# Kernel tuning notes

Hardware: AMD Instinct MI355X
Metric: run time of the kernel (lower is better)

Reference implementation:

```python
import jax, jax.numpy as jnp
import numpy as np

B, S, P = 256, 1024, 4096   # batch, n_sensors, n_points
NM, H, PD = 64, 128, 128    # n_modes, hidden width, p
C = 1.0                     # speed of light param


def setup_inputs() -> dict:
    key = jax.random.key(0)
    ks = jax.random.split(key, 16)
    w = lambda k, shp: (jax.random.normal(k, shp, jnp.float32) * 0.05)
    return {
        "u0": jax.random.normal(ks[0], (B, S), jnp.float32),
        "x": jax.random.uniform(ks[1], (P,), jnp.float32, -1.0, 1.0),
        "t": jax.random.uniform(ks[2], (P,), jnp.float32, 0.0, 1.0),
        # branch MLP: (2*NM)->128->128->PD
        "bw1": w(ks[3], (H, 2 * NM)), "bb1": jnp.zeros((H,), jnp.float32),
        "bw2": w(ks[4], (H, H)),      "bb2": jnp.zeros((H,), jnp.float32),
        "bw3": w(ks[5], (PD, H)),     "bb3": jnp.zeros((PD,), jnp.float32),
        # trunk MLP: 4->128->128->PD
        "tw1": w(ks[6], (H, 4)),      "tb1": jnp.zeros((H,), jnp.float32),
        "tw2": w(ks[7], (H, H)),      "tb2": jnp.zeros((H,), jnp.float32),
        "tw3": w(ks[8], (PD, H)),     "tb3": jnp.zeros((PD,), jnp.float32),
    }


def _mlp(a, w1, b1, w2, b2, w3, b3):
    a = jax.nn.relu(a @ w1.T + b1)
    a = jax.nn.relu(a @ w2.T + b2)
    return a @ w3.T + b3


def reference(u0, x, t, bw1, bb1, bw2, bb2, bw3, bb3, tw1, tb1, tw2, tb2, tw3, tb3):
    # Fourier coefficients: mean over sensors of u0 * cos/sin(pi*k*xs)
    xs = jnp.linspace(-1.0, 1.0, S, dtype=jnp.float32)          # (S,)
    modes = jnp.arange(1, NM + 1, dtype=jnp.float32)            # (NM,)
    ang = jnp.pi * modes[:, None] * xs[None, :]                 # (NM, S)
    cos_c = (u0 @ jnp.cos(ang).T) / S                           # (B, NM)
    sin_c = (u0 @ jnp.sin(ang).T) / S                           # (B, NM)
    fourier = jnp.concatenate([cos_c, sin_c], axis=1)           # (B, 2*NM)

    branch_out = _mlp(fourier, bw1, bb1, bw2, bb2, bw3, bb3)    # (B, PD)

    xe = jnp.broadcast_to(x[None, :], (u0.shape[0], P))         # (B, P)
    te = jnp.broadcast_to(t[None, :], (u0.shape[0], P))
    pt_sq = te ** 2 - xe ** 2 / (C ** 2)
    # safe sqrt of clamp(pt_sq, min=0)
    proper_time = jnp.sqrt(jnp.where(pt_sq > 0, pt_sq, 0.0) + 0.0)
    causal = (jnp.abs(xe) <= C * te).astype(jnp.float32)
    trunk_feat = jnp.stack([xe, te, proper_time, causal], axis=-1)  # (B, P, 4)

    trunk_out = _mlp(trunk_feat, tw1, tb1, tw2, tb2, tw3, tb3)      # (B, P, PD)

    u_pred = jnp.einsum("bd,bpd->bp", branch_out, trunk_out)        # (B, P)
    return u_pred * causal
```

## Files before the change

### kernel.cpp

```cpp
#include <hip/hip_runtime.h>
#include <hip/hip_fp16.h>
#include <math.h>

#define NMODES 64
#define SDIM   1024
#define BATCH  256
#define PDIM   4096
#define HDIM   128

typedef _Float16 half8  __attribute__((ext_vector_type(8)));
typedef _Float16 half4v __attribute__((ext_vector_type(4)));
typedef float    f32x4  __attribute__((ext_vector_type(4)));

#define WSB_BRANCH 0
#define WSB_T3     (BATCH * HDIM * 2)

#define LDW 136

union KMixSmem {
    struct {
        _Float16 Ws[128 * LDW];
        _Float16 h1[32 * LDW];
        _Float16 h2[32 * LDW];
        float    feat[32][4];
    } tr;
    struct {
        float u0row[SDIM];
        float part[2][HDIM];
        float fr[HDIM];
        float hh[HDIM];
        float g2[HDIM];
    } fb;
};

__global__ __launch_bounds__(256) void k_mix(
    const float* __restrict__ u0,
    const float* __restrict__ xv, const float* __restrict__ tv,
    const float* __restrict__ bw1, const float* __restrict__ bb1,
    const float* __restrict__ bw2, const float* __restrict__ bb2,
    const float* __restrict__ bw3, const float* __restrict__ bb3,
    const float* __restrict__ tw1, const float* __restrict__ tb1,
    const float* __restrict__ tw2, const float* __restrict__ tb2,
    const float* __restrict__ tw3, const float* __restrict__ tb3,
    __half* __restrict__ branch_out, __half* __restrict__ t3g) {
    __shared__ KMixSmem sm;
    const int t = threadIdx.x;

    if (blockIdx.x < 128) {
        const int pbase = blockIdx.x * 32;

#pragma unroll
        for (int i = 0; i < 16; ++i) {
            int F = i * 256 + t;
            float4 wv = ((const float4*)tw2)[F];
            half4v h; h.x = (_Float16)wv.x; h.y = (_Float16)wv.y;
            h.z = (_Float16)wv.z; h.w = (_Float16)wv.w;
            *(half4v*)&sm.tr.Ws[(F >> 5) * LDW + (F & 31) * 4] = h;
        }
        if (t < 32) {
            int p = pbase + t;
            float x = xv[p], tt = tv[p];
            float qq = tt * tt - x * x;
            sm.tr.feat[t][0] = x;
            sm.tr.feat[t][1] = tt;
            sm.tr.feat[t][2] = (qq > 0.f) ? sqrtf(qq) : 0.f;
            sm.tr.feat[t][3] = (fabsf(x) <= tt) ? 1.f : 0.f;
        }
        __syncthreads();

        const int j = t & 127, pg = t >> 7;
        {
            float4 w1 = ((const float4*)tw1)[j];
            float b1 = tb1[j];
#pragma unroll
            for (int i = 0; i < 16; ++i) {
                int p = 2 * i + pg;
                float4 f = *(const float4*)sm.tr.feat[p];
                float v = fmaf(w1.x, f.x, fmaf(w1.y, f.y,
                           fmaf(w1.z, f.z, fmaf(w1.w, f.w, b1))));
                sm.tr.h1[p * LDW + j] = (_Float16)fmaxf(v, 0.f);
            }
        }
        __syncthreads();

        const int lane = t & 63, w = t >> 6;
        const int lm = lane & 15, q = lane >> 4;
        const int mt = w & 1, nh = w >> 1;

        {
            f32x4 acc[4] = {f32x4{0,0,0,0}, f32x4{0,0,0,0},
                            f32x4{0,0,0,0}, f32x4{0,0,0,0}};
            const _Float16* aB = &sm.tr.h1[(mt * 16 + lm) * LDW + q * 8];
#pragma unroll
            for (int ks = 0; ks < 4; ++ks) {
                half8 af = *(const half8*)(aB + ks * 32);
#pragma unroll
                for (int n = 0; n < 4; ++n) {
                    half8 bf = *(const half8*)
                        &sm.tr.Ws[((nh * 4 + n) * 16 + lm) * LDW + q * 8 + ks * 32];
                    acc[n] = __builtin_amdgcn_mfma_f32_16x16x32_f16(af, bf, acc[n], 0, 0, 0);
                }
            }
#pragma unroll
            for (int n = 0; n < 4; ++n) {
                int col = (nh * 4 + n) * 16 + lm;
                float b = tb2[col];
#pragma unroll
                for (int e = 0; e < 4; ++e)
                    sm.tr.h2[(mt * 16 + q * 4 + e) * LDW + col] =
                        (_Float16)fmaxf(acc[n][e] + b, 0.f);
            }
        }
        __syncthreads();

#pragma unroll
        for (int i = 0; i < 16; ++i) {
            int F = i * 256 + t;
            float4 wv = ((const float4*)tw3)[F];
            half4v h; h.x = (_Float16)wv.x; h.y = (_Float16)wv.y;
            h.z = (_Float16)wv.z; h.w = (_Float16)wv.w;
            *(half4v*)&sm.tr.Ws[(F >> 5) * LDW + (F & 31) * 4] = h;
        }
        __syncthreads();

        {
            f32x4 acc[4] = {f32x4{0,0,0,0}, f32x4{0,0,0,0},
                            f32x4{0,0,0,0}, f32x4{0,0,0,0}};
            const _Float16* aB = &sm.tr.h2[(mt * 16 + lm) * LDW + q * 8];
#pragma unroll
            for (int ks = 0; ks < 4; ++ks) {
                half8 af = *(const half8*)(aB + ks * 32);
#pragma unroll
                for (int n = 0; n < 4; ++n) {
                    half8 bf = *(const half8*)
                        &sm.tr.Ws[((nh * 4 + n) * 16 + lm) * LDW + q * 8 + ks * 32];
                    acc[n] = __builtin_amdgcn_mfma_f32_16x16x32_f16(af, bf, acc[n], 0, 0, 0);
                }
            }
#pragma unroll
            for (int n = 0; n < 4; ++n) {
                int col = (nh * 4 + n) * 16 + lm;
                float b = tb3[col];
#pragma unroll
                for (int e = 0; e < 4; ++e) {
                    int p = pbase + mt * 16 + q * 4 + e;
                    t3g[(size_t)p * HDIM + col] = __float2half(acc[n][e] + b);
                }
            }
        }
        return;
    }

    const int row = blockIdx.x - 128;
    ((float4*)sm.fb.u0row)[t] = ((const float4*)(u0 + (size_t)row * SDIM))[t];
    __syncthreads();

    const int j = t & 127, sh = t >> 7;
    {
        const int kmode = (j & 63) + 1;
        const float r  = (float)kmode * (1.0f / 1023.0f);
        const float a0 = -0.5f * (float)kmode;
        float sf = (float)(sh * 512);
        const float* up = sm.fb.u0row + sh * 512;
        float acc = 0.f;
        if (j < 64) {
#pragma unroll 8
            for (int s = 0; s < 512; ++s) {
                float a = fmaf(sf, r, a0);
                a -= floorf(a);
                acc = fmaf(__builtin_amdgcn_cosf(a), up[s], acc);
                sf += 1.0f;
            }
        } else {
#pragma unroll 8
            for (int s = 0; s < 512; ++s) {
                float a = fmaf(sf, r, a0);
                a -= floorf(a);
                acc = fmaf(__builtin_amdgcn_sinf(a), up[s], acc);
                sf += 1.0f;
            }
        }
        sm.fb.part[sh][j] = acc;
    }
    __syncthreads();
    if (t < 128)
        sm.fb.fr[j] = (sm.fb.part[0][j] + sm.fb.part[1][j]) * (1.0f / (float)SDIM);
    __syncthreads();

    if (t < 128) {
        const float4* wp = (const float4*)(bw1 + (size_t)j * HDIM);
        float c0 = bb1[j];
        for (int i4 = 0; i4 < 32; ++i4) {
            float4 wv = wp[i4];
            float4 x0 = *(const float4*)&sm.fb.fr[i4 * 4];
            c0 += wv.x * x0.x + wv.y * x0.y + wv.z * x0.z + wv.w * x0.w;
        }
        sm.fb.hh[j] = fmaxf(c0, 0.f);
    }
    __syncthreads();
    if (t < 128) {
        const float4* wp = (const float4*)(bw2 + (size_t)j * HDIM);
        float c0 = bb2[j];
        for (int i4 = 0; i4 < 32; ++i4) {
            float4 wv = wp[i4];
            float4 x0 = *(const float4*)&sm.fb.hh[i4 * 4];
            c0 += wv.x * x0.x + wv.y * x0.y + wv.z * x0.z + wv.w * x0.w;
        }
        sm.fb.g2[j] = fmaxf(c0, 0.f);
    }
    __syncthreads();
    if (t < 128) {
        const float4* wp = (const float4*)(bw3 + (size_t)j * HDIM);
        float c0 = bb3[j];
        for (int i4 = 0; i4 < 32; ++i4) {
            float4 wv = wp[i4];
            float4 x0 = *(const float4*)&sm.fb.g2[i4 * 4];
            c0 += wv.x * x0.x + wv.y * x0.y + wv.z * x0.z + wv.w * x0.w;
        }
        branch_out[(size_t)row * HDIM + j] = __float2half(c0);
    }
}

#define LDH 136
__global__ __launch_bounds__(256) void k_final(
    const __half* __restrict__ br_g, const __half* __restrict__ t3g,
    const float* __restrict__ xv, const float* __restrict__ tv,
    float* __restrict__ out) {
    __shared__ _Float16 brL[64 * LDH];
    __shared__ _Float16 ttL[64 * LDH];
    __shared__ float causL[64];

    const int t = threadIdx.x;
    const int rb = blockIdx.x >> 6;
    const int cb = blockIdx.x & 63;

    if (t < 64) {
        int p = cb * 64 + t;
        float x = xv[p], tt = tv[p];
        causL[t] = (fabsf(x) <= tt) ? 1.f : 0.f;
    }

#pragma unroll
    for (int it = 0; it < 4; ++it) {
        int flat = t + 256 * it;
        int row = flat >> 4, c = flat & 15;
        *(float4*)&brL[row * LDH + c * 8] =
            *(const float4*)&br_g[(size_t)(rb * 64 + row) * HDIM + c * 8];
        *(float4*)&ttL[row * LDH + c * 8] =
            *(const float4*)&t3g[(size_t)(cb * 64 + row) * HDIM + c * 8];
    }
    __syncthreads();

    const int lane = t & 63;
    const int w = t >> 6;
    const int lm = lane & 15;
    const int q = lane >> 4;

    f32x4 acc[4] = {f32x4{0,0,0,0}, f32x4{0,0,0,0}, f32x4{0,0,0,0}, f32x4{0,0,0,0}};

    const _Float16* aBase = &brL[(16 * w + lm) * LDH + q * 8];
#pragma unroll
    for (int ks = 0; ks < 4; ++ks) {
        half8 af = *(const half8*)(aBase + ks * 32);
#pragma unroll
        for (int jt = 0; jt < 4; ++jt) {
            half8 bf = *(const half8*)&ttL[(16 * jt + lm) * LDH + q * 8 + ks * 32];
            acc[jt] = __builtin_amdgcn_mfma_f32_16x16x32_f16(af, bf, acc[jt], 0, 0, 0);
        }
    }

#pragma unroll
    for (int jt = 0; jt < 4; ++jt) {
        int col = cb * 64 + 16 * jt + lm;
        float cz = causL[16 * jt + lm];
#pragma unroll
        for (int e = 0; e < 4; ++e) {
            int row = rb * 64 + 16 * w + q * 4 + e;
            out[(size_t)row * PDIM + col] = acc[jt][e] * cz;
        }
    }
}

extern "C" void kernel_launch(void* const* d_in, const int* in_sizes, int n_in,
                              void* d_out, int out_size, void* d_ws, size_t ws_size,
                              hipStream_t stream) {
    const float* u0  = (const float*)d_in[0];
    const float* xv  = (const float*)d_in[1];
    const float* tv  = (const float*)d_in[2];
    const float* bw1 = (const float*)d_in[3];
    const float* bb1 = (const float*)d_in[4];
    const float* bw2 = (const float*)d_in[5];
    const float* bb2 = (const float*)d_in[6];
    const float* bw3 = (const float*)d_in[7];
    const float* bb3 = (const float*)d_in[8];
    const float* tw1 = (const float*)d_in[9];
    const float* tb1 = (const float*)d_in[10];
    const float* tw2 = (const float*)d_in[11];
    const float* tb2 = (const float*)d_in[12];
    const float* tw3 = (const float*)d_in[13];
    const float* tb3 = (const float*)d_in[14];

    char* wsb = (char*)d_ws;
    __half* branch_out = (__half*)(wsb + WSB_BRANCH);
    __half* t3g        = (__half*)(wsb + WSB_T3);
    float* out = (float*)d_out;

    hipLaunchKernelGGL(k_mix, dim3(384), dim3(256), 0, stream,
                       u0, xv, tv, bw1, bb1, bw2, bb2, bw3, bb3,
                       tw1, tb1, tw2, tb2, tw3, tb3, branch_out, t3g);
    hipLaunchKernelGGL(k_final, dim3(256), dim3(256), 0, stream,
                       branch_out, t3g, xv, tv, out);
}
```

Measured before the change: 103.0 us.

## Fuse branch, trunk and final contraction into one cooperative kernel with grid sync

Replaces the two-kernel pipeline with a single cooperative launch of 256 blocks of 512 threads. Each block computes one batch row's branch MLP, then a grid-wide sync publishes branch_out. Each block then computes a 16-point trunk MLP tile and directly forms the final 256x16 output slice using MFMA, reading branch_out from global memory. This removes a kernel launch and the t3 round trip through global memory. In exchange it adds a grid barrier, uses a smaller per-block tile with less MFMA reuse, and relies on all 256 blocks being co-resident.

```diff
diff --git a/kernel.cpp b/kernel.cpp
--- a/kernel.cpp
+++ b/kernel.cpp
@@ -1,6 +1,9 @@
 #include <hip/hip_runtime.h>
+#include <hip/hip_cooperative_groups.h>
 #include <hip/hip_fp16.h>
 #include <math.h>
+
+namespace cg = cooperative_groups;
 
 #define NMODES 64
 #define SDIM   1024
@@ -12,28 +15,10 @@
 typedef _Float16 half4v __attribute__((ext_vector_type(4)));
 typedef float    f32x4  __attribute__((ext_vector_type(4)));
 
-#define WSB_BRANCH 0
-#define WSB_T3     (BATCH * HDIM * 2)
-
 #define LDW 136
 
-union KMixSmem {
-    struct {
-        _Float16 Ws[128 * LDW];
-        _Float16 h1[32 * LDW];
-        _Float16 h2[32 * LDW];
-        float    feat[32][4];
-    } tr;
-    struct {
-        float u0row[SDIM];
-        float part[2][HDIM];
-        float fr[HDIM];
-        float hh[HDIM];
-        float g2[HDIM];
-    } fb;
-};
-
-__global__ __launch_bounds__(256) void k_mix(
+
+__global__ __launch_bounds__(512, 1) void k_all(
     const float* __restrict__ u0,
     const float* __restrict__ xv, const float* __restrict__ tv,
     const float* __restrict__ bw1, const float* __restrict__ bb1,
@@ -42,130 +27,60 @@
     const float* __restrict__ tw1, const float* __restrict__ tb1,
     const float* __restrict__ tw2, const float* __restrict__ tb2,
     const float* __restrict__ tw3, const float* __restrict__ tb3,
-    __half* __restrict__ branch_out, __half* __restrict__ t3g) {
-    __shared__ KMixSmem sm;
+    __half* __restrict__ branch_out, float* __restrict__ out) {
+    __shared__ _Float16 Ws[128 * LDW];
+    __shared__ _Float16 t3L[16 * LDW];
+    __shared__ float    feat[16][4];
+    __shared__ union {
+        struct {
+            float u0row[SDIM];
+            float part[4][HDIM];
+            float fr[HDIM];
+            float hh[HDIM];
+            float g2[HDIM];
+        } fb;
+        struct {
+            _Float16 h1[16 * LDW];
+            _Float16 h2[16 * LDW];
+        } tr;
+    } ax;
+
     const int t = threadIdx.x;
-
-    if (blockIdx.x < 128) {
-        const int pbase = blockIdx.x * 32;
-
-#pragma unroll
-        for (int i = 0; i < 16; ++i) {
-            int F = i * 256 + t;
-            float4 wv = ((const float4*)tw2)[F];
-            half4v h; h.x = (_Float16)wv.x; h.y = (_Float16)wv.y;
-            h.z = (_Float16)wv.z; h.w = (_Float16)wv.w;
-            *(half4v*)&sm.tr.Ws[(F >> 5) * LDW + (F & 31) * 4] = h;
-        }
-        if (t < 32) {
-            int p = pbase + t;
-            float x = xv[p], tt = tv[p];
-            float qq = tt * tt - x * x;
-            sm.tr.feat[t][0] = x;
-            sm.tr.feat[t][1] = tt;
-            sm.tr.feat[t][2] = (qq > 0.f) ? sqrtf(qq) : 0.f;
-            sm.tr.feat[t][3] = (fabsf(x) <= tt) ? 1.f : 0.f;
-        }
-        __syncthreads();
-
-        const int j = t & 127, pg = t >> 7;
-        {
-            float4 w1 = ((const float4*)tw1)[j];
-            float b1 = tb1[j];
-#pragma unroll
-            for (int i = 0; i < 16; ++i) {
-                int p = 2 * i + pg;
-                float4 f = *(const float4*)sm.tr.feat[p];
-                float v = fmaf(w1.x, f.x, fmaf(w1.y, f.y,
-                           fmaf(w1.z, f.z, fmaf(w1.w, f.w, b1))));
-                sm.tr.h1[p * LDW + j] = (_Float16)fmaxf(v, 0.f);
-            }
-        }
-        __syncthreads();
-
-        const int lane = t & 63, w = t >> 6;
-        const int lm = lane & 15, q = lane >> 4;
-        const int mt = w & 1, nh = w >> 1;
-
-        {
-            f32x4 acc[4] = {f32x4{0,0,0,0}, f32x4{0,0,0,0},
-                            f32x4{0,0,0,0}, f32x4{0,0,0,0}};
-            const _Float16* aB = &sm.tr.h1[(mt * 16 + lm) * LDW + q * 8];
-#pragma unroll
-            for (int ks = 0; ks < 4; ++ks) {
-                half8 af = *(const half8*)(aB + ks * 32);
-#pragma unroll
-                for (int n = 0; n < 4; ++n) {
-                    half8 bf = *(const half8*)
-                        &sm.tr.Ws[((nh * 4 + n) * 16 + lm) * LDW + q * 8 + ks * 32];
-                    acc[n] = __builtin_amdgcn_mfma_f32_16x16x32_f16(af, bf, acc[n], 0, 0, 0);
-                }
-            }
-#pragma unroll
-            for (int n = 0; n < 4; ++n) {
-                int col = (nh * 4 + n) * 16 + lm;
-                float b = tb2[col];
-#pragma unroll
-                for (int e = 0; e < 4; ++e)
-                    sm.tr.h2[(mt * 16 + q * 4 + e) * LDW + col] =
-                        (_Float16)fmaxf(acc[n][e] + b, 0.f);
-            }
-        }
-        __syncthreads();
-
-#pragma unroll
-        for (int i = 0; i < 16; ++i) {
-            int F = i * 256 + t;
-            float4 wv = ((const float4*)tw3)[F];
-            half4v h; h.x = (_Float16)wv.x; h.y = (_Float16)wv.y;
-            h.z = (_Float16)wv.z; h.w = (_Float16)wv.w;
-            *(half4v*)&sm.tr.Ws[(F >> 5) * LDW + (F & 31) * 4] = h;
-        }
-        __syncthreads();
-
-        {
-            f32x4 acc[4] = {f32x4{0,0,0,0}, f32x4{0,0,0,0},
-                            f32x4{0,0,0,0}, f32x4{0,0,0,0}};
-            const _Float16* aB = &sm.tr.h2[(mt * 16 + lm) * LDW + q * 8];
-#pragma unroll
-            for (int ks = 0; ks < 4; ++ks) {
-                half8 af = *(const half8*)(aB + ks * 32);
-#pragma unroll
-                for (int n = 0; n < 4; ++n) {
-                    half8 bf = *(const half8*)
-                        &sm.tr.Ws[((nh * 4 + n) * 16 + lm) * LDW + q * 8 + ks * 32];
-                    acc[n] = __builtin_amdgcn_mfma_f32_16x16x32_f16(af, bf, acc[n], 0, 0, 0);
-                }
-            }
-#pragma unroll
-            for (int n = 0; n < 4; ++n) {
-                int col = (nh * 4 + n) * 16 + lm;
-                float b = tb3[col];
-#pragma unroll
-                for (int e = 0; e < 4; ++e) {
-                    int p = pbase + mt * 16 + q * 4 + e;
-                    t3g[(size_t)p * HDIM + col] = __float2half(acc[n][e] + b);
-                }
-            }
-        }
-        return;
-    }
-
-    const int row = blockIdx.x - 128;
-    ((float4*)sm.fb.u0row)[t] = ((const float4*)(u0 + (size_t)row * SDIM))[t];
-    __syncthreads();
-
-    const int j = t & 127, sh = t >> 7;
-    {
+    const int b = blockIdx.x;
+    const int pbase = b * 16;
+
+    if (t < 256)
+        ((float4*)ax.fb.u0row)[t] = ((const float4*)(u0 + (size_t)b * SDIM))[t];
+#pragma unroll
+    for (int i = 0; i < 8; ++i) {
+        int F = i * 512 + t;
+        float4 wv = ((const float4*)tw2)[F];
+        half4v h; h.x = (_Float16)wv.x; h.y = (_Float16)wv.y;
+        h.z = (_Float16)wv.z; h.w = (_Float16)wv.w;
+        *(half4v*)&Ws[(F >> 5) * LDW + (F & 31) * 4] = h;
+    }
+    if (t < 16) {
+        int p = pbase + t;
+        float x = xv[p], tt = tv[p];
+        float qq = tt * tt - x * x;
+        feat[t][0] = x;
+        feat[t][1] = tt;
+        feat[t][2] = (qq > 0.f) ? sqrtf(qq) : 0.f;
+        feat[t][3] = (fabsf(x) <= tt) ? 1.f : 0.f;
+    }
+    __syncthreads();
+
+    {
+        const int j = t & 127, sh = t >> 7;
         const int kmode = (j & 63) + 1;
         const float r  = (float)kmode * (1.0f / 1023.0f);
         const float a0 = -0.5f * (float)kmode;
-        float sf = (float)(sh * 512);
-        const float* up = sm.fb.u0row + sh * 512;
+        float sf = (float)(sh * 256);
+        const float* up = ax.fb.u0row + sh * 256;
         float acc = 0.f;
-        if (j < 64) {
+        if ((j & 64) == 0) {
 #pragma unroll 8
-            for (int s = 0; s < 512; ++s) {
+            for (int s = 0; s < 256; ++s) {
                 float a = fmaf(sf, r, a0);
                 a -= floorf(a);
                 acc = fmaf(__builtin_amdgcn_cosf(a), up[s], acc);
@@ -173,110 +88,138 @@
             }
         } else {
 #pragma unroll 8
-            for (int s = 0; s < 512; ++s) {
+            for (int s = 0; s < 256; ++s) {
                 float a = fmaf(sf, r, a0);
                 a -= floorf(a);
                 acc = fmaf(__builtin_amdgcn_sinf(a), up[s], acc);
                 sf += 1.0f;
             }
         }
-        sm.fb.part[sh][j] = acc;
+        ax.fb.part[sh][j] = acc;
     }
     __syncthreads();
     if (t < 128)
-        sm.fb.fr[j] = (sm.fb.part[0][j] + sm.fb.part[1][j]) * (1.0f / (float)SDIM);
+        ax.fb.fr[t] = (ax.fb.part[0][t] + ax.fb.part[1][t] +
+                       ax.fb.part[2][t] + ax.fb.part[3][t]) * (1.0f / (float)SDIM);
     __syncthreads();
 
     if (t < 128) {
-        const float4* wp = (const float4*)(bw1 + (size_t)j * HDIM);
-        float c0 = bb1[j];
+        const float4* wp = (const float4*)(bw1 + (size_t)t * HDIM);
+        float c0 = bb1[t];
         for (int i4 = 0; i4 < 32; ++i4) {
             float4 wv = wp[i4];
-            float4 x0 = *(const float4*)&sm.fb.fr[i4 * 4];
+            float4 x0 = *(const float4*)&ax.fb.fr[i4 * 4];
             c0 += wv.x * x0.x + wv.y * x0.y + wv.z * x0.z + wv.w * x0.w;
         }
-        sm.fb.hh[j] = fmaxf(c0, 0.f);
+        ax.fb.hh[t] = fmaxf(c0, 0.f);
     }
     __syncthreads();
     if (t < 128) {
-        const float4* wp = (const float4*)(bw2 + (size_t)j * HDIM);
-        float c0 = bb2[j];
+        const float4* wp = (const float4*)(bw2 + (size_t)t * HDIM);
+        float c0 = bb2[t];
         for (int i4 = 0; i4 < 32; ++i4) {
             float4 wv = wp[i4];
-            float4 x0 = *(const float4*)&sm.fb.hh[i4 * 4];
+            float4 x0 = *(const float4*)&ax.fb.hh[i4 * 4];
             c0 += wv.x * x0.x + wv.y * x0.y + wv.z * x0.z + wv.w * x0.w;
         }
-        sm.fb.g2[j] = fmaxf(c0, 0.f);
+        ax.fb.g2[t] = fmaxf(c0, 0.f);
     }
     __syncthreads();
     if (t < 128) {
-        const float4* wp = (const float4*)(bw3 + (size_t)j * HDIM);
-        float c0 = bb3[j];
+        const float4* wp = (const float4*)(bw3 + (size_t)t * HDIM);
+        float c0 = bb3[t];
         for (int i4 = 0; i4 < 32; ++i4) {
             float4 wv = wp[i4];
-            float4 x0 = *(const float4*)&sm.fb.g2[i4 * 4];
+            float4 x0 = *(const float4*)&ax.fb.g2[i4 * 4];
             c0 += wv.x * x0.x + wv.y * x0.y + wv.z * x0.z + wv.w * x0.w;
         }
-        branch_out[(size_t)row * HDIM + j] = __float2half(c0);
-    }
-}
-
-#define LDH 136
-__global__ __launch_bounds__(256) void k_final(
-    const __half* __restrict__ br_g, const __half* __restrict__ t3g,
-    const float* __restrict__ xv, const float* __restrict__ tv,
-    float* __restrict__ out) {
-    __shared__ _Float16 brL[64 * LDH];
-    __shared__ _Float16 ttL[64 * LDH];
-    __shared__ float causL[64];
-
-    const int t = threadIdx.x;
-    const int rb = blockIdx.x >> 6;
-    const int cb = blockIdx.x & 63;
-
-    if (t < 64) {
-        int p = cb * 64 + t;
-        float x = xv[p], tt = tv[p];
-        causL[t] = (fabsf(x) <= tt) ? 1.f : 0.f;
-    }
-
-#pragma unroll
-    for (int it = 0; it < 4; ++it) {
-        int flat = t + 256 * it;
-        int row = flat >> 4, c = flat & 15;
-        *(float4*)&brL[row * LDH + c * 8] =
-            *(const float4*)&br_g[(size_t)(rb * 64 + row) * HDIM + c * 8];
-        *(float4*)&ttL[row * LDH + c * 8] =
-            *(const float4*)&t3g[(size_t)(cb * 64 + row) * HDIM + c * 8];
-    }
-    __syncthreads();
-
-    const int lane = t & 63;
-    const int w = t >> 6;
-    const int lm = lane & 15;
-    const int q = lane >> 4;
-
-    f32x4 acc[4] = {f32x4{0,0,0,0}, f32x4{0,0,0,0}, f32x4{0,0,0,0}, f32x4{0,0,0,0}};
-
-    const _Float16* aBase = &brL[(16 * w + lm) * LDH + q * 8];
-#pragma unroll
-    for (int ks = 0; ks < 4; ++ks) {
-        half8 af = *(const half8*)(aBase + ks * 32);
-#pragma unroll
-        for (int jt = 0; jt < 4; ++jt) {
-            half8 bf = *(const half8*)&ttL[(16 * jt + lm) * LDH + q * 8 + ks * 32];
-            acc[jt] = __builtin_amdgcn_mfma_f32_16x16x32_f16(af, bf, acc[jt], 0, 0, 0);
-        }
-    }
-
-#pragma unroll
-    for (int jt = 0; jt < 4; ++jt) {
-        int col = cb * 64 + 16 * jt + lm;
-        float cz = causL[16 * jt + lm];
+        branch_out[(size_t)b * HDIM + t] = __float2half(c0);
+    }
+    __threadfence();
+    cg::this_grid().sync();
+
+    {
+        const int j = t & 127, p0 = t >> 7;
+        float4 w1 = ((const float4*)tw1)[j];
+        float b1 = tb1[j];
+#pragma unroll
+        for (int i = 0; i < 4; ++i) {
+            int p = i * 4 + p0;
+            float4 f = *(const float4*)feat[p];
+            float v = fmaf(w1.x, f.x, fmaf(w1.y, f.y,
+                       fmaf(w1.z, f.z, fmaf(w1.w, f.w, b1))));
+            ax.tr.h1[p * LDW + j] = (_Float16)fmaxf(v, 0.f);
+        }
+    }
+    __syncthreads();
+
+    const int lane = t & 63, w = t >> 6;
+    const int lm = lane & 15, q = lane >> 4;
+
+    {
+        f32x4 acc = {0.f, 0.f, 0.f, 0.f};
+        const _Float16* aB = &ax.tr.h1[lm * LDW + q * 8];
+        const _Float16* bB = &Ws[(w * 16 + lm) * LDW + q * 8];
+#pragma unroll
+        for (int ks = 0; ks < 4; ++ks) {
+            half8 af = *(const half8*)(aB + ks * 32);
+            half8 bf = *(const half8*)(bB + ks * 32);
+            acc = __builtin_amdgcn_mfma_f32_16x16x32_f16(af, bf, acc, 0, 0, 0);
+        }
+        int col = w * 16 + lm;
+        float bias = tb2[col];
+#pragma unroll
+        for (int e = 0; e < 4; ++e)
+            ax.tr.h2[(q * 4 + e) * LDW + col] = (_Float16)fmaxf(acc[e] + bias, 0.f);
+    }
+    __syncthreads();
+
+#pragma unroll
+    for (int i = 0; i < 8; ++i) {
+        int F = i * 512 + t;
+        float4 wv = ((const float4*)tw3)[F];
+        half4v h; h.x = (_Float16)wv.x; h.y = (_Float16)wv.y;
+        h.z = (_Float16)wv.z; h.w = (_Float16)wv.w;
+        *(half4v*)&Ws[(F >> 5) * LDW + (F & 31) * 4] = h;
+    }
+    __syncthreads();
+
+    {
+        f32x4 acc = {0.f, 0.f, 0.f, 0.f};
+        const _Float16* aB = &ax.tr.h2[lm * LDW + q * 8];
+        const _Float16* bB = &Ws[(w * 16 + lm) * LDW + q * 8];
+#pragma unroll
+        for (int ks = 0; ks < 4; ++ks) {
+            half8 af = *(const half8*)(aB + ks * 32);
+            half8 bf = *(const half8*)(bB + ks * 32);
+            acc = __builtin_amdgcn_mfma_f32_16x16x32_f16(af, bf, acc, 0, 0, 0);
+        }
+        int col = w * 16 + lm;
+        float bias = tb3[col];
+#pragma unroll
+        for (int e = 0; e < 4; ++e)
+            t3L[(q * 4 + e) * LDW + col] = (_Float16)(acc[e] + bias);
+    }
+    __syncthreads();
+
+    {
+        float x = xv[pbase + lm], tt = tv[pbase + lm];
+        float cz = (fabsf(x) <= tt) ? 1.f : 0.f;
+        const _Float16* brp = (const _Float16*)branch_out;
+        f32x4 acc0 = {0.f, 0.f, 0.f, 0.f};
+        f32x4 acc1 = {0.f, 0.f, 0.f, 0.f};
+#pragma unroll
+        for (int ks = 0; ks < 4; ++ks) {
+            half8 bf  = *(const half8*)&t3L[lm * LDW + q * 8 + ks * 32];
+            half8 af0 = *(const half8*)&brp[(size_t)(w * 32 + lm) * HDIM + q * 8 + ks * 32];
+            half8 af1 = *(const half8*)&brp[(size_t)(w * 32 + 16 + lm) * HDIM + q * 8 + ks * 32];
+            acc0 = __builtin_amdgcn_mfma_f32_16x16x32_f16(af0, bf, acc0, 0, 0, 0);
+            acc1 = __builtin_amdgcn_mfma_f32_16x16x32_f16(af1, bf, acc1, 0, 0, 0);
+        }
 #pragma unroll
         for (int e = 0; e < 4; ++e) {
-            int row = rb * 64 + 16 * w + q * 4 + e;
-            out[(size_t)row * PDIM + col] = acc[jt][e] * cz;
+            out[(size_t)(w * 32 + q * 4 + e) * PDIM + pbase + lm]      = acc0[e] * cz;
+            out[(size_t)(w * 32 + 16 + q * 4 + e) * PDIM + pbase + lm] = acc1[e] * cz;
         }
     }
 }
@@ -300,14 +243,17 @@
     const float* tw3 = (const float*)d_in[13];
     const float* tb3 = (const float*)d_in[14];
 
-    char* wsb = (char*)d_ws;
-    __half* branch_out = (__half*)(wsb + WSB_BRANCH);
-    __half* t3g        = (__half*)(wsb + WSB_T3);
+    __half* branch_out = (__half*)d_ws;
     float* out = (float*)d_out;
 
-    hipLaunchKernelGGL(k_mix, dim3(384), dim3(256), 0, stream,
-                       u0, xv, tv, bw1, bb1, bw2, bb2, bw3, bb3,
-                       tw1, tb1, tw2, tb2, tw3, tb3, branch_out, t3g);
-    hipLaunchKernelGGL(k_final, dim3(256), dim3(256), 0, stream,
-                       branch_out, t3g, xv, tv, out);
+    void* args[] = {
+        (void*)&u0, (void*)&xv, (void*)&tv,
+        (void*)&bw1, (void*)&bb1, (void*)&bw2, (void*)&bb2,
+        (void*)&bw3, (void*)&bb3,
+        (void*)&tw1, (void*)&tb1, (void*)&tw2, (void*)&tb2,
+        (void*)&tw3, (void*)&tb3,
+        (void*)&branch_out, (void*)&out,
+    };
+    hipLaunchCooperativeKernel((const void*)k_all, dim3(256), dim3(512),
+                               args, 0, stream);
 }
```

Result: slower. 181.0 us (+75.8%).
